# Kernel tuning notes

Measured on AMD Instinct MI355X. Metric: run time of the kernel, lower is better.

## Reference

```python
import jax, jax.numpy as jnp
import numpy as np

B, S, D, R, H = 4, 2048, 1024, 256, 8
NI, NP, NO, K = 8, 32, 8, 3
DH = R // H


def _householder_chain(x, vs):
    # x: [B,S,R], vs: [B,S,K,R]; apply K Householder reflections sequentially
    def step(carry, v):
        vn = v * jax.lax.rsqrt(jnp.sum(v * v, axis=-1, keepdims=True) + 1e-8)
        vTx = jnp.sum(carry * vn, axis=-1, keepdims=True)
        return carry - 2.0 * vn * vTx, None
    out, _ = jax.lax.scan(step, x, jnp.moveaxis(vs, 2, 0))
    return out


def _circuit_down(x, in_neurons, proc_neurons, input_weights, proc_idx):
    # soft mixture of input-neuron projections: d_model -> rank
    all_proj = jnp.einsum('bsd,ndr->bsnr', x, in_neurons)
    xr = jnp.einsum('bsnr,bsn->bsr', all_proj, input_weights)
    return _householder_chain(xr, proc_neurons[proc_idx])


def setup_inputs():
    key = jax.random.key(0)
    ks = jax.random.split(key, 14)
    n = lambda k, shape, sc: jax.random.normal(k, shape, jnp.float32) * sc
    inv_d, inv_r = 1.0 / np.sqrt(D), 1.0 / np.sqrt(R)
    return {
        'x': n(ks[0], (B, S, D), 1.0),
        'q_in': n(ks[1], (NI, D, R), inv_d),
        'q_proc': n(ks[2], (NP, R), inv_r),
        'k_in': n(ks[3], (NI, D, R), inv_d),
        'k_proc': n(ks[4], (NP, R), inv_r),
        'v_in': n(ks[5], (NI, D, R), inv_d),
        'v_proc': n(ks[6], (NP, R), inv_r),
        'o_proc': n(ks[7], (NP, R), inv_r),
        'o_out': n(ks[8], (NO, R, D), inv_r),
        'rd_in': n(ks[9], (NI, D), inv_d),
        'rd_proc': n(ks[10], (NP, D), inv_d),
        'ru_out': n(ks[11], (NO, R), inv_r),
        'ru_proc': n(ks[12], (NP, R), inv_r),
    }


def reference(x, q_in, q_proc, k_in, k_proc, v_in, v_proc, o_proc, o_out,
              rd_in, rd_proc, ru_out, ru_proc):
    # --- router (down): soft input weights + top-k process indices ---
    input_weights = jax.nn.softmax(x @ rd_in.T, axis=-1)          # [B,S,NI]
    _, pidx = jax.lax.top_k(x @ rd_proc.T, K)                     # [B,S,K]

    q = _circuit_down(x, q_in, q_proc, input_weights, pidx)      # [B,S,R]
    k = _circuit_down(x, k_in, k_proc, input_weights, pidx)
    v = _circuit_down(x, v_in, v_proc, input_weights, pidx)

    qh = q.reshape(B, S, H, DH)
    kh = k.reshape(B, S, H, DH)
    vh = v.reshape(B, S, H, DH)
    scores = jnp.einsum('bqhd,bkhd->bhqk', qh, kh) / np.sqrt(DH)
    attn = jax.nn.softmax(scores, axis=-1)
    o = jnp.einsum('bhqk,bkhd->bqhd', attn, vh).reshape(B, S, R)  # [B,S,R]

    # --- router (up): soft output weights + top-k process indices ---
    output_weights = jax.nn.softmax(o @ ru_out.T, axis=-1)        # [B,S,NO]
    _, pidx_u = jax.lax.top_k(o @ ru_proc.T, K)                   # [B,S,K]

    oh = _householder_chain(o, o_proc[pidx_u])                    # [B,S,R]
    out = jnp.einsum('bsr,bsn,nrd->bsd', oh, output_weights, o_out)
    return out
```

## Files before the change

kernel.cpp:

```cpp
#include <hip/hip_runtime.h>
#include <math.h>

#define NI 8
#define NP 32
#define TOPK 3

typedef _Float16 f16;
typedef f16 f16x8 __attribute__((ext_vector_type(8)));
typedef f16 f16x4 __attribute__((ext_vector_type(4)));
typedef float f32x4 __attribute__((ext_vector_type(4)));

__device__ __forceinline__ float wave_sum(float v) {
  #pragma unroll
  for (int off = 32; off; off >>= 1) v += __shfl_xor(v, off);
  return v;
}

__device__ __forceinline__ unsigned int pack_f16x2(float x) {
  f16 h = (f16)x;
  f16 l = (f16)(x - (float)h);
  return (unsigned int)__builtin_bit_cast(unsigned short, h)
       | ((unsigned int)__builtin_bit_cast(unsigned short, l) << 16);
}

__device__ __forceinline__ void unpack8(const unsigned int* p, f16x8& hi, f16x8& lo) {
  uint4 w0 = *reinterpret_cast<const uint4*>(p);
  uint4 w1 = *reinterpret_cast<const uint4*>(p + 4);
  union { unsigned int u[4]; f16x8 v; } H, L;
  H.u[0] = (w0.x & 0xffffu) | (w0.y << 16);
  L.u[0] = (w0.x >> 16)     | (w0.y & 0xffff0000u);
  H.u[1] = (w0.z & 0xffffu) | (w0.w << 16);
  L.u[1] = (w0.z >> 16)     | (w0.w & 0xffff0000u);
  H.u[2] = (w1.x & 0xffffu) | (w1.y << 16);
  L.u[2] = (w1.x >> 16)     | (w1.y & 0xffff0000u);
  H.u[3] = (w1.z & 0xffffu) | (w1.w << 16);
  L.u[3] = (w1.z >> 16)     | (w1.w & 0xffff0000u);
  hi = H.v; lo = L.v;
}

template<int CHUNKS>
__global__ __launch_bounds__(256) void router_kernel(
    const float* __restrict__ X,
    const float* __restrict__ Wsm,
    const float* __restrict__ Wtk,
    float* __restrict__ iw, int* __restrict__ pidx)
{
  const int tid = threadIdx.x, wave = tid >> 6, lane = tid & 63;
  const int t = blockIdx.x * 4 + wave;
  __shared__ float sc[4][40];
  const int Kin = CHUNKS * 256;
  const float4* Xp = reinterpret_cast<const float4*>(X + (size_t)t * Kin);
  float4 xv[CHUNKS];
  #pragma unroll
  for (int c = 0; c < CHUNKS; ++c) xv[c] = Xp[c * 64 + lane];

  for (int w = 0; w < 40; ++w) {
    const float* Wr = (w < NI) ? (Wsm + (size_t)w * Kin) : (Wtk + (size_t)(w - NI) * Kin);
    const float4* Wp = reinterpret_cast<const float4*>(Wr);
    float p = 0.f;
    #pragma unroll
    for (int c = 0; c < CHUNKS; ++c) {
      float4 wv = Wp[c * 64 + lane];
      p = fmaf(xv[c].x, wv.x, p); p = fmaf(xv[c].y, wv.y, p);
      p = fmaf(xv[c].z, wv.z, p); p = fmaf(xv[c].w, wv.w, p);
    }
    p = wave_sum(p);
    if (lane == 0) sc[wave][w] = p;
  }
  float s = (lane < NI) ? sc[wave][lane] : -3.0e38f;
  float m = s;
  #pragma unroll
  for (int off = 4; off; off >>= 1) m = fmaxf(m, __shfl_xor(m, off));
  float e = expf(s - m);
  float sum = e;
  #pragma unroll
  for (int off = 4; off; off >>= 1) sum += __shfl_xor(sum, off);
  if (lane < NI) iw[(size_t)t * NI + lane] = e / sum;

  float v = (lane < NP) ? sc[wave][NI + lane] : -3.0e38f;
  int idx = lane;
  #pragma unroll
  for (int j = 0; j < TOPK; ++j) {
    float bv = v; int bi = idx;
    #pragma unroll
    for (int off = 32; off; off >>= 1) {
      float ov = __shfl_xor(bv, off); int oi = __shfl_xor(bi, off);
      if (ov > bv || (ov == bv && oi < bi)) { bv = ov; bi = oi; }
    }
    if (lane == 0) pidx[t * TOPK + j] = bi;
    if (idx == bi) v = -3.0e38f;
  }
}

__global__ __launch_bounds__(256) void pack_bt(
    const float* __restrict__ S, f16* __restrict__ Dh, f16* __restrict__ Dl,
    int C, int K)
{
  __shared__ float T[64][65];
  const int tid = threadIdx.x;
  const int kb = blockIdx.x * 64, cb = blockIdx.y * 64;
  const int tr = tid >> 4, tc = (tid & 15) * 4;
  #pragma unroll
  for (int i = 0; i < 4; ++i) {
    float4 v = *reinterpret_cast<const float4*>(&S[(size_t)(kb + tr + i * 16) * C + cb + tc]);
    T[tr + i * 16][tc + 0] = v.x; T[tr + i * 16][tc + 1] = v.y;
    T[tr + i * 16][tc + 2] = v.z; T[tr + i * 16][tc + 3] = v.w;
  }
  __syncthreads();
  #pragma unroll
  for (int i = 0; i < 4; ++i) {
    int c = tr + i * 16;
    f16x4 vh, vl;
    #pragma unroll
    for (int q = 0; q < 4; ++q) {
      float a = T[tc + q][c];
      f16 h = (f16)a;
      vh[q] = h;
      vl[q] = (f16)(a - (float)h);
    }
    *reinterpret_cast<f16x4*>(&Dh[(size_t)(cb + c) * K + kb + tc]) = vh;
    *reinterpret_cast<f16x4*>(&Dl[(size_t)(cb + c) * K + kb + tc]) = vl;
  }
}

#define SBM 128
#define SBN 64
#define SBK 32

__global__ __launch_bounds__(256, 3) void gemm_split(
    const float* __restrict__ X, int Kin,
    const float* __restrict__ W,
    const f16* __restrict__ Bth, const f16* __restrict__ Btl,
    float* __restrict__ C, int ldC, int Ktot)
{
  __shared__ f16x8 AhU[SBM * 4];
  __shared__ f16x8 AlU[SBM * 4];
  __shared__ f16x8 BhU[SBN * 4];
  __shared__ f16x8 BlU[SBN * 4];
  __shared__ float Ws[SBM][NI];

  const int tid = threadIdx.x;
  const int row0 = blockIdx.x * SBM;
  const int c0 = blockIdx.y * SBN;

  const int wave = tid >> 6, lane = tid & 63;
  const int wm = wave >> 1, wn = wave & 1;
  const int fr = lane & 15, ks = lane >> 4;

  for (int i = tid; i < SBM * NI; i += 256)
    Ws[i >> 3][i & 7] = W[(size_t)(row0 + (i >> 3)) * NI + (i & 7)];

  const int arow = tid >> 1, ahalf = tid & 1;
  const float* xrow = X + (size_t)(row0 + arow) * Kin + ahalf * 16;
  const int bcol = tid >> 2;
  const int bks = (tid & 3) ^ (bcol & 3);
  const f16* bsh = Bth + (size_t)(c0 + bcol) * Ktot + bks * 8;
  const f16* bsl = Btl + (size_t)(c0 + bcol) * Ktot + bks * 8;

  f32x4 acc[4][2] = {};

  int n = 0, dk0 = 0;
  for (int kt = 0; kt < Ktot; kt += SBK) {
    __syncthreads();
    {
      float4 v0 = *reinterpret_cast<const float4*>(xrow + dk0);
      float4 v1 = *reinterpret_cast<const float4*>(xrow + dk0 + 4);
      float4 v2 = *reinterpret_cast<const float4*>(xrow + dk0 + 8);
      float4 v3 = *reinterpret_cast<const float4*>(xrow + dk0 + 12);
      float wgt = Ws[arow][n];
      float a[16] = {v0.x, v0.y, v0.z, v0.w, v1.x, v1.y, v1.z, v1.w,
                     v2.x, v2.y, v2.z, v2.w, v3.x, v3.y, v3.z, v3.w};
      f16x8 h0, h1, l0, l1;
      #pragma unroll
      for (int j = 0; j < 8; ++j) {
        float p0 = a[j] * wgt, p1 = a[8 + j] * wgt;
        f16 hh0 = (f16)p0, hh1 = (f16)p1;
        h0[j] = hh0; l0[j] = (f16)(p0 - (float)hh0);
        h1[j] = hh1; l1[j] = (f16)(p1 - (float)hh1);
      }
      const int sw = arow & 3;
      AhU[arow * 4 + ((ahalf * 2 + 0) ^ sw)] = h0;
      AhU[arow * 4 + ((ahalf * 2 + 1) ^ sw)] = h1;
      AlU[arow * 4 + ((ahalf * 2 + 0) ^ sw)] = l0;
      AlU[arow * 4 + ((ahalf * 2 + 1) ^ sw)] = l1;
      BhU[tid] = *reinterpret_cast<const f16x8*>(bsh + kt);
      BlU[tid] = *reinterpret_cast<const f16x8*>(bsl + kt);
    }
    __syncthreads();
    f16x8 ah[4], al[4], bh[2], bl[2];
    #pragma unroll
    for (int mf = 0; mf < 4; ++mf) {
      int ar = wm * 64 + mf * 16 + fr;
      int s = ar * 4 + (ks ^ (ar & 3));
      ah[mf] = AhU[s]; al[mf] = AlU[s];
    }
    #pragma unroll
    for (int nf = 0; nf < 2; ++nf) {
      int bc = wn * 32 + nf * 16 + fr;
      int s = bc * 4 + (ks ^ (bc & 3));
      bh[nf] = BhU[s]; bl[nf] = BlU[s];
    }
    #pragma unroll
    for (int mf = 0; mf < 4; ++mf)
      #pragma unroll
      for (int nf = 0; nf < 2; ++nf) {
        acc[mf][nf] = __builtin_amdgcn_mfma_f32_16x16x32_f16(ah[mf], bh[nf], acc[mf][nf], 0, 0, 0);
        acc[mf][nf] = __builtin_amdgcn_mfma_f32_16x16x32_f16(ah[mf], bl[nf], acc[mf][nf], 0, 0, 0);
        acc[mf][nf] = __builtin_amdgcn_mfma_f32_16x16x32_f16(al[mf], bh[nf], acc[mf][nf], 0, 0, 0);
      }
    dk0 += SBK;
    if (dk0 == Kin) { dk0 = 0; ++n; }
  }
  #pragma unroll
  for (int mf = 0; mf < 4; ++mf)
    #pragma unroll
    for (int nf = 0; nf < 2; ++nf) {
      int col = c0 + wn * 32 + nf * 16 + fr;
      #pragma unroll
      for (int j = 0; j < 4; ++j) {
        int row = row0 + wm * 64 + mf * 16 + ks * 4 + j;
        C[(size_t)row * ldC + col] = acc[mf][nf][j];
      }
    }
}

#define GBM 128
#define GBN 128
#define GBK 16
#define GBMp 132

__global__ __launch_bounds__(256) void gemm_mix(
    const float* __restrict__ X, int Kin,
    const float* __restrict__ W,
    const float* __restrict__ Bm0, const float* __restrict__ Bm1, const float* __restrict__ Bm2,
    int ldB, float* __restrict__ C, int ldC, int Nz)
{
  __shared__ float As[GBK][GBMp];
  __shared__ float Bs[GBK][GBMp];
  __shared__ float Ws[GBM][NI];
  const int tid = threadIdx.x;
  const int row0 = blockIdx.x * GBM;
  const int z = blockIdx.z;
  const float* Bm = (z == 0) ? Bm0 : (z == 1) ? Bm1 : Bm2;
  const int c0 = blockIdx.y * GBN;
  for (int i = tid; i < GBM * NI; i += 256)
    Ws[i >> 3][i & 7] = W[(size_t)(row0 + (i >> 3)) * NI + (i & 7)];
  __syncthreads();

  float acc[8][8] = {};
  const int tr = tid >> 4, tc = tid & 15;
  const int srow = tid >> 2;
  const int sseg = (tid & 3) * 4;
  const int bk = tid >> 4;
  const int bc = (tid & 15) * 4;

  const int Ktot = Kin * NI;
  int n = 0, dk0 = 0;
  for (int kt = 0; kt < Ktot; kt += GBK) {
    __syncthreads();
    #pragma unroll
    for (int p = 0; p < 2; ++p) {
      int r = p * 64 + srow;
      float4 xv = *reinterpret_cast<const float4*>(&X[(size_t)(row0 + r) * Kin + dk0 + sseg]);
      float wgt = Ws[r][n];
      As[sseg + 0][r] = xv.x * wgt;
      As[sseg + 1][r] = xv.y * wgt;
      As[sseg + 2][r] = xv.z * wgt;
      As[sseg + 3][r] = xv.w * wgt;
    }
    #pragma unroll
    for (int p = 0; p < 2; ++p) {
      int cc = p * 64 + bc;
      float4 bv = *reinterpret_cast<const float4*>(&Bm[(size_t)(kt + bk) * ldB + c0 + cc]);
      *reinterpret_cast<float4*>(&Bs[bk][cc]) = bv;
    }
    __syncthreads();
    #pragma unroll
    for (int k = 0; k < GBK; ++k) {
      float4 a0 = *reinterpret_cast<const float4*>(&As[k][tr * 8]);
      float4 a1 = *reinterpret_cast<const float4*>(&As[k][tr * 8 + 4]);
      float4 b0 = *reinterpret_cast<const float4*>(&Bs[k][tc * 8]);
      float4 b1 = *reinterpret_cast<const float4*>(&Bs[k][tc * 8 + 4]);
      float av[8] = {a0.x, a0.y, a0.z, a0.w, a1.x, a1.y, a1.z, a1.w};
      float bv[8] = {b0.x, b0.y, b0.z, b0.w, b1.x, b1.y, b1.z, b1.w};
      #pragma unroll
      for (int i = 0; i < 8; ++i)
        #pragma unroll
        for (int j = 0; j < 8; ++j)
          acc[i][j] = fmaf(av[i], bv[j], acc[i][j]);
    }
    dk0 += GBK;
    if (dk0 == Kin) { dk0 = 0; ++n; }
  }
  #pragma unroll
  for (int i = 0; i < 8; ++i) {
    int row = row0 + tr * 8 + i;
    float* Cp = C + (size_t)row * ldC + z * Nz + c0 + tc * 8;
    float4 o0 = {acc[i][0], acc[i][1], acc[i][2], acc[i][3]};
    float4 o1 = {acc[i][4], acc[i][5], acc[i][6], acc[i][7]};
    *reinterpret_cast<float4*>(Cp) = o0;
    *reinterpret_cast<float4*>(Cp + 4) = o1;
  }
}

__global__ __launch_bounds__(256) void hh_kernel(
    float* __restrict__ X, int ldX,
    const float* __restrict__ P0, const float* __restrict__ P1, const float* __restrict__ P2,
    const int* __restrict__ pidx)
{
  const int tid = threadIdx.x, wave = tid >> 6, lane = tid & 63;
  const int t = blockIdx.x * 4 + wave;
  const int circ = blockIdx.y;
  const float* P = (circ == 0) ? P0 : (circ == 1) ? P1 : P2;
  float* xp = X + (size_t)t * ldX + circ * 256;
  float4 x4 = *reinterpret_cast<float4*>(xp + lane * 4);
  #pragma unroll
  for (int j = 0; j < TOPK; ++j) {
    int id = pidx[t * TOPK + j];
    const float* vp = P + (size_t)id * 256;
    float4 v4 = *reinterpret_cast<const float4*>(vp + lane * 4);
    float ss = v4.x * v4.x + v4.y * v4.y + v4.z * v4.z + v4.w * v4.w;
    ss = wave_sum(ss);
    float inv = 1.0f / sqrtf(ss + 1e-8f);
    float4 vn = {v4.x * inv, v4.y * inv, v4.z * inv, v4.w * inv};
    float dt = vn.x * x4.x + vn.y * x4.y + vn.z * x4.z + vn.w * x4.w;
    dt = wave_sum(dt);
    float d2 = 2.0f * dt;
    x4.x = fmaf(-d2, vn.x, x4.x);
    x4.y = fmaf(-d2, vn.y, x4.y);
    x4.z = fmaf(-d2, vn.z, x4.z);
    x4.w = fmaf(-d2, vn.w, x4.w);
  }
  *reinterpret_cast<float4*>(xp + lane * 4) = x4;
}

__global__ __launch_bounds__(256, 2) void attn_mfma(
    const float* __restrict__ qkv, float* __restrict__ O)
{
  __shared__ f16 Kh[64][40];
  __shared__ f16 Kl[64][40];
  __shared__ unsigned int Vtp[32][68];
  __shared__ unsigned int Pp[4][32][68];

  const int tid = threadIdx.x, wave = tid >> 6, lane = tid & 63;
  const int c = lane & 15, g = lane >> 4;
  const int bh = blockIdx.y, b = bh >> 3, h = bh & 7;
  const int q0 = blockIdx.x * 128;
  const size_t tbase = (size_t)b * 2048;
  const float SCALE = 0.17677669529663687f;

  f16x8 qh[2], ql[2];
  #pragma unroll
  for (int qt = 0; qt < 2; ++qt) {
    const int row = q0 + wave * 32 + qt * 16 + c;
    const float* qp = qkv + (tbase + row) * 768 + h * 32 + g * 8;
    float4 a = *reinterpret_cast<const float4*>(qp);
    float4 b4 = *reinterpret_cast<const float4*>(qp + 4);
    float qv[8] = {a.x, a.y, a.z, a.w, b4.x, b4.y, b4.z, b4.w};
    #pragma unroll
    for (int j = 0; j < 8; ++j) {
      float xs = qv[j] * SCALE;
      f16 hh = (f16)xs;
      qh[qt][j] = hh;
      ql[qt][j] = (f16)(xs - (float)hh);
    }
  }

  f32x4 sacc[2][4];
  f32x4 oacc[2][2] = {};
  float mrow[2][4] = {{-INFINITY, -INFINITY, -INFINITY, -INFINITY},
                      {-INFINITY, -INFINITY, -INFINITY, -INFINITY}};
  float lrow[2][4] = {};

  for (int k0 = 0; k0 < 2048; k0 += 64) {
    __syncthreads();
    {
      const int kj = tid >> 2, dq = (tid & 3) * 8;
      const float* kp = qkv + (tbase + k0 + kj) * 768 + 256 + h * 32 + dq;
      float4 ka = *reinterpret_cast<const float4*>(kp);
      float4 kb = *reinterpret_cast<const float4*>(kp + 4);
      float kv[8] = {ka.x, ka.y, ka.z, ka.w, kb.x, kb.y, kb.z, kb.w};
      f16x8 khi, klo;
      #pragma unroll
      for (int j = 0; j < 8; ++j) {
        f16 hh = (f16)kv[j];
        khi[j] = hh;
        klo[j] = (f16)(kv[j] - (float)hh);
      }
      *reinterpret_cast<f16x8*>(&Kh[kj][dq]) = khi;
      *reinterpret_cast<f16x8*>(&Kl[kj][dq]) = klo;

      const int vk = tid & 63, vq = (tid >> 6) * 8;
      const float* vp = qkv + (tbase + k0 + vk) * 768 + 512 + h * 32 + vq;
      float4 va = *reinterpret_cast<const float4*>(vp);
      float4 vb = *reinterpret_cast<const float4*>(vp + 4);
      float vv[8] = {va.x, va.y, va.z, va.w, vb.x, vb.y, vb.z, vb.w};
      #pragma unroll
      for (int j = 0; j < 8; ++j) Vtp[vq + j][vk] = pack_f16x2(vv[j]);
    }
    __syncthreads();

    #pragma unroll
    for (int s = 0; s < 4; ++s) {
      f16x8 kbh = *reinterpret_cast<const f16x8*>(&Kh[s * 16 + c][g * 8]);
      f16x8 kbl = *reinterpret_cast<const f16x8*>(&Kl[s * 16 + c][g * 8]);
      #pragma unroll
      for (int qt = 0; qt < 2; ++qt) {
        f32x4 acc = {0.f, 0.f, 0.f, 0.f};
        acc = __builtin_amdgcn_mfma_f32_16x16x32_f16(qh[qt], kbh, acc, 0, 0, 0);
        acc = __builtin_amdgcn_mfma_f32_16x16x32_f16(qh[qt], kbl, acc, 0, 0, 0);
        acc = __builtin_amdgcn_mfma_f32_16x16x32_f16(ql[qt], kbh, acc, 0, 0, 0);
        sacc[qt][s] = acc;
      }
    }

    float alpha[2][4];
    #pragma unroll
    for (int qt = 0; qt < 2; ++qt)
      #pragma unroll
      for (int r = 0; r < 4; ++r) {
        float mt = fmaxf(fmaxf(sacc[qt][0][r], sacc[qt][1][r]),
                         fmaxf(sacc[qt][2][r], sacc[qt][3][r]));
        #pragma unroll
        for (int off = 1; off < 16; off <<= 1) mt = fmaxf(mt, __shfl_xor(mt, off));
        float mn = fmaxf(mrow[qt][r], mt);
        float al = __expf(mrow[qt][r] - mn);
        mrow[qt][r] = mn;
        alpha[qt][r] = al;
        float ps = 0.f;
        #pragma unroll
        for (int s = 0; s < 4; ++s) {
          float p = __expf(sacc[qt][s][r] - mn);
          sacc[qt][s][r] = p;
          ps += p;
        }
        #pragma unroll
        for (int off = 1; off < 16; off <<= 1) ps += __shfl_xor(ps, off);
        lrow[qt][r] = lrow[qt][r] * al + ps;
      }

    #pragma unroll
    for (int qt = 0; qt < 2; ++qt)
      #pragma unroll
      for (int s = 0; s < 4; ++s)
        #pragma unroll
        for (int r = 0; r < 4; ++r)
          Pp[wave][qt * 16 + g * 4 + r][s * 16 + c] = pack_f16x2(sacc[qt][s][r]);

    #pragma unroll
    for (int qt = 0; qt < 2; ++qt)
      #pragma unroll
      for (int dh = 0; dh < 2; ++dh)
        #pragma unroll
        for (int r = 0; r < 4; ++r) oacc[qt][dh][r] *= alpha[qt][r];

    #pragma unroll
    for (int ch = 0; ch < 2; ++ch) {
      f16x8 pah[2], pal[2];
      #pragma unroll
      for (int qt = 0; qt < 2; ++qt)
        unpack8(&Pp[wave][qt * 16 + c][ch * 32 + g * 8], pah[qt], pal[qt]);
      #pragma unroll
      for (int dh = 0; dh < 2; ++dh) {
        f16x8 vh, vl;
        unpack8(&Vtp[dh * 16 + c][ch * 32 + g * 8], vh, vl);
        #pragma unroll
        for (int qt = 0; qt < 2; ++qt) {
          oacc[qt][dh] = __builtin_amdgcn_mfma_f32_16x16x32_f16(pah[qt], vh, oacc[qt][dh], 0, 0, 0);
          oacc[qt][dh] = __builtin_amdgcn_mfma_f32_16x16x32_f16(pah[qt], vl, oacc[qt][dh], 0, 0, 0);
          oacc[qt][dh] = __builtin_amdgcn_mfma_f32_16x16x32_f16(pal[qt], vh, oacc[qt][dh], 0, 0, 0);
        }
      }
    }
  }

  #pragma unroll
  for (int qt = 0; qt < 2; ++qt)
    #pragma unroll
    for (int r = 0; r < 4; ++r) {
      float inv = 1.0f / lrow[qt][r];
      int row = q0 + wave * 32 + qt * 16 + g * 4 + r;
      #pragma unroll
      for (int dh = 0; dh < 2; ++dh)
        O[(tbase + row) * 256 + h * 32 + dh * 16 + c] = oacc[qt][dh][r] * inv;
    }
}

__global__ __launch_bounds__(256) void attn_kernel(
    const float* __restrict__ qkv, float* __restrict__ O)
{
  const int tid = threadIdx.x;
  const int wave = tid >> 6, lane = tid & 63;
  const int bh = blockIdx.y, b = bh >> 3, h = bh & 7;
  const int q0 = blockIdx.x * 8;
  const size_t tbase = (size_t)b * 2048;
  const float SCALE = 0.17677669529663687f;

  __shared__ float Ks[64][36];
  __shared__ float Vt[32][68];
  __shared__ float Ps[4][2][64];

  const int wq = __builtin_amdgcn_readfirstlane(wave);
  const float* qr0 = qkv + (tbase + q0 + wq * 2) * 768 + h * 32;
  float qa[32], qb[32];
  #pragma unroll
  for (int i = 0; i < 32; ++i) { qa[i] = qr0[i]; qb[i] = qr0[768 + i]; }

  const int r = lane >> 5, d = lane & 31;
  float m0 = -INFINITY, m1 = -INFINITY, l0 = 0.f, l1 = 0.f, oacc = 0.f;

  for (int k0 = 0; k0 < 2048; k0 += 64) {
    __syncthreads();
    {
      int j = tid >> 2;
      int c = (tid & 3) * 8;
      const float* kp = qkv + (tbase + k0 + j) * 768 + 256 + h * 32 + c;
      float4 ka = *reinterpret_cast<const float4*>(kp);
      float4 kb = *reinterpret_cast<const float4*>(kp + 4);
      *reinterpret_cast<float4*>(&Ks[j][c]) = ka;
      *reinterpret_cast<float4*>(&Ks[j][c + 4]) = kb;
      const float* vp = qkv + (tbase + k0 + j) * 768 + 512 + h * 32 + c;
      float4 va = *reinterpret_cast<const float4*>(vp);
      float4 vb = *reinterpret_cast<const float4*>(vp + 4);
      Vt[c + 0][j] = va.x; Vt[c + 1][j] = va.y; Vt[c + 2][j] = va.z; Vt[c + 3][j] = va.w;
      Vt[c + 4][j] = vb.x; Vt[c + 5][j] = vb.y; Vt[c + 6][j] = vb.z; Vt[c + 7][j] = vb.w;
    }
    __syncthreads();
    float s0 = 0.f, s1 = 0.f;
    #pragma unroll
    for (int dd = 0; dd < 8; ++dd) {
      float4 kv = *reinterpret_cast<const float4*>(&Ks[lane][dd * 4]);
      s0 = fmaf(qa[dd * 4 + 0], kv.x, s0); s1 = fmaf(qb[dd * 4 + 0], kv.x, s1);
      s0 = fmaf(qa[dd * 4 + 1], kv.y, s0); s1 = fmaf(qb[dd * 4 + 1], kv.y, s1);
      s0 = fmaf(qa[dd * 4 + 2], kv.z, s0); s1 = fmaf(qb[dd * 4 + 2], kv.z, s1);
      s0 = fmaf(qa[dd * 4 + 3], kv.w, s0); s1 = fmaf(qb[dd * 4 + 3], kv.w, s1);
    }
    s0 *= SCALE; s1 *= SCALE;
    float mx0 = s0, mx1 = s1;
    #pragma unroll
    for (int off = 32; off; off >>= 1) {
      mx0 = fmaxf(mx0, __shfl_xor(mx0, off));
      mx1 = fmaxf(mx1, __shfl_xor(mx1, off));
    }
    float nm0 = fmaxf(m0, mx0), nm1 = fmaxf(m1, mx1);
    float p0 = expf(s0 - nm0), p1 = expf(s1 - nm1);
    float a0 = expf(m0 - nm0), a1 = expf(m1 - nm1);
    float sp0 = p0, sp1 = p1;
    #pragma unroll
    for (int off = 32; off; off >>= 1) {
      sp0 += __shfl_xor(sp0, off);
      sp1 += __shfl_xor(sp1, off);
    }
    l0 = l0 * a0 + sp0; l1 = l1 * a1 + sp1;
    m0 = nm0; m1 = nm1;
    Ps[wave][0][lane] = p0; Ps[wave][1][lane] = p1;
    oacc *= (r == 0) ? a0 : a1;
    #pragma unroll
    for (int jq = 0; jq < 16; ++jq) {
      float4 pv = *reinterpret_cast<const float4*>(&Ps[wave][r][jq * 4]);
      float4 vv = *reinterpret_cast<const float4*>(&Vt[d][jq * 4]);
      oacc = fmaf(pv.x, vv.x, oacc);
      oacc = fmaf(pv.y, vv.y, oacc);
      oacc = fmaf(pv.z, vv.z, oacc);
      oacc = fmaf(pv.w, vv.w, oacc);
    }
  }
  float lf = (r == 0) ? l0 : l1;
  oacc /= lf;
  O[(tbase + q0 + wave * 2 + r) * 256 + h * 32 + d] = oacc;
}

extern "C" void kernel_launch(void* const* d_in, const int* in_sizes, int n_in,
                              void* d_out, int out_size, void* d_ws, size_t ws_size,
                              hipStream_t stream) {
  const float* x       = (const float*)d_in[0];
  const float* q_in    = (const float*)d_in[1];
  const float* q_proc  = (const float*)d_in[2];
  const float* k_in    = (const float*)d_in[3];
  const float* k_proc  = (const float*)d_in[4];
  const float* v_in    = (const float*)d_in[5];
  const float* v_proc  = (const float*)d_in[6];
  const float* o_proc  = (const float*)d_in[7];
  const float* o_out   = (const float*)d_in[8];
  const float* rd_in   = (const float*)d_in[9];
  const float* rd_proc = (const float*)d_in[10];
  const float* ru_out  = (const float*)d_in[11];
  const float* ru_proc = (const float*)d_in[12];
  float* out = (float*)d_out;
  float* qkv = (float*)d_out;

  const size_t NEED = (768ull << 10) + 768ull * 8192 * 2 * 2;

  if (ws_size >= NEED) {
    char* wsb = (char*)d_ws;
    float* iw    = (float*)wsb;
    float* owt   = (float*)(wsb + (256 << 10));
    int*   pidx  = (int*)(wsb + (512 << 10));
    int*   pidxu = (int*)(wsb + (640 << 10));
    char*  Xr    = wsb + (768 << 10);
    f16* bth_q = (f16*)Xr;
    f16* btl_q = (f16*)(Xr + 768ull * 8192 * 2);
    float* obuf = (float*)Xr;
    f16* bth_o = (f16*)(Xr + (8ull << 20));
    f16* btl_o = (f16*)(Xr + (8ull << 20) + 1024ull * 2048 * 2);

    router_kernel<4><<<dim3(2048), dim3(256), 0, stream>>>(x, rd_in, rd_proc, iw, pidx);
    pack_bt<<<dim3(128, 4), dim3(256), 0, stream>>>(q_in, bth_q,                btl_q,                256, 8192);
    pack_bt<<<dim3(128, 4), dim3(256), 0, stream>>>(k_in, bth_q + 256ull * 8192, btl_q + 256ull * 8192, 256, 8192);
    pack_bt<<<dim3(128, 4), dim3(256), 0, stream>>>(v_in, bth_q + 512ull * 8192, btl_q + 512ull * 8192, 256, 8192);
    gemm_split<<<dim3(64, 12), dim3(256), 0, stream>>>(x, 1024, iw, bth_q, btl_q, qkv, 768, 8192);
    hh_kernel<<<dim3(2048, 3), dim3(256), 0, stream>>>(qkv, 768, q_proc, k_proc, v_proc, pidx);
    pack_bt<<<dim3(32, 16), dim3(256), 0, stream>>>(o_out, bth_o, btl_o, 1024, 2048);
    attn_mfma<<<dim3(16, 32), dim3(256), 0, stream>>>(qkv, obuf);
    router_kernel<1><<<dim3(2048), dim3(256), 0, stream>>>(obuf, ru_out, ru_proc, owt, pidxu);
    hh_kernel<<<dim3(2048, 1), dim3(256), 0, stream>>>(obuf, 256, o_proc, o_proc, o_proc, pidxu);
    gemm_split<<<dim3(64, 16), dim3(256), 0, stream>>>(obuf, 256, owt, bth_o, btl_o, out, 1024, 2048);
  } else {
    float* ws = (float*)d_ws;
    float* iw    = ws;
    int*   pidx  = (int*)(ws + 65536);
    float* obuf  = ws + 65536 + 24576;
    float* owt   = obuf + 8192 * 256;
    int*   pidxu = (int*)(owt + 65536);

    router_kernel<4><<<dim3(2048), dim3(256), 0, stream>>>(x, rd_in, rd_proc, iw, pidx);
    gemm_mix<<<dim3(64, 2, 3), dim3(256), 0, stream>>>(x, 1024, iw, q_in, k_in, v_in,
                                                       256, qkv, 768, 256);
    hh_kernel<<<dim3(2048, 3), dim3(256), 0, stream>>>(qkv, 768, q_proc, k_proc, v_proc, pidx);
    attn_kernel<<<dim3(256, 32), dim3(256), 0, stream>>>(qkv, obuf);
    router_kernel<1><<<dim3(2048), dim3(256), 0, stream>>>(obuf, ru_out, ru_proc, owt, pidxu);
    hh_kernel<<<dim3(2048, 1), dim3(256), 0, stream>>>(obuf, 256, o_proc, o_proc, o_proc, pidxu);
    gemm_mix<<<dim3(64, 8, 1), dim3(256), 0, stream>>>(obuf, 256, owt, o_out, o_out, o_out,
                                                       1024, out, 1024, 1024);
  }
}
```

Before: 823.6 us.

## Pre-split activations to f16 hi/lo and use async LDS-load GEMM with larger tiles

```diff
diff --git a/kernel.cpp b/kernel.cpp
--- a/kernel.cpp
+++ b/kernel.cpp
@@ -14,6 +14,12 @@
   #pragma unroll
   for (int off = 32; off; off >>= 1) v += __shfl_xor(v, off);
   return v;
+}
+
+__device__ __forceinline__ void gload16(const void* g, void* l) {
+  __builtin_amdgcn_global_load_lds(
+      (const __attribute__((address_space(1))) unsigned int*)g,
+      (__attribute__((address_space(3))) unsigned int*)l, 16, 0, 0);
 }
 
 __device__ __forceinline__ unsigned int pack_f16x2(float x) {
@@ -121,6 +127,143 @@
     *reinterpret_cast<f16x4*>(&Dh[(size_t)(cb + c) * K + kb + tc]) = vh;
     *reinterpret_cast<f16x4*>(&Dl[(size_t)(cb + c) * K + kb + tc]) = vl;
   }
+}
+
+__global__ __launch_bounds__(256) void pack_split(
+    const float* __restrict__ S, f16* __restrict__ Dh, f16* __restrict__ Dl,
+    size_t n8)
+{
+  size_t i = ((size_t)blockIdx.x * 256 + threadIdx.x);
+  if (i >= n8) return;
+  const float* s = S + i * 8;
+  float4 a = *reinterpret_cast<const float4*>(s);
+  float4 b = *reinterpret_cast<const float4*>(s + 4);
+  float v[8] = {a.x, a.y, a.z, a.w, b.x, b.y, b.z, b.w};
+  f16x8 h, l;
+  #pragma unroll
+  for (int j = 0; j < 8; ++j) {
+    f16 hh = (f16)v[j];
+    h[j] = hh;
+    l[j] = (f16)(v[j] - (float)hh);
+  }
+  *reinterpret_cast<f16x8*>(Dh + i * 8) = h;
+  *reinterpret_cast<f16x8*>(Dl + i * 8) = l;
+}
+
+#define TBM 128
+#define TBN 128
+#define TBK 32
+
+__global__ __launch_bounds__(256, 2) void gemm_split2(
+    const f16* __restrict__ Xh, const f16* __restrict__ Xl, int Kin,
+    const float* __restrict__ W,
+    const f16* __restrict__ Bth, const f16* __restrict__ Btl,
+    float* __restrict__ C, int ldC, int Ktot)
+{
+  __shared__ f16x8 AhL[512];
+  __shared__ f16x8 AlL[512];
+  __shared__ f16x8 BhL[512];
+  __shared__ f16x8 BlL[512];
+  __shared__ float Ws[TBM][NI];
+
+  const int tid = threadIdx.x;
+  const int wave = tid >> 6, lane = tid & 63;
+  const int wm = wave >> 1, wn = wave & 1;
+  const int fr = lane & 15, ks = lane >> 4;
+  const int row0 = blockIdx.x * TBM, c0 = blockIdx.y * TBN;
+
+  for (int i = tid; i < TBM * NI; i += 256)
+    Ws[i >> 3][i & 7] = W[(size_t)(row0 + (i >> 3)) * NI + (i & 7)];
+
+  const int s1 = 256 + tid;
+  const int ar0 = tid >> 2, kg0 = ((tid & 3) - (ar0 >> 1)) & 3;
+  const int ar1 = s1 >> 2,  kg1 = ((s1 & 3) - (ar1 >> 1)) & 3;
+
+  const f16* xh0 = Xh + (size_t)(row0 + ar0) * Kin + kg0 * 8;
+  const f16* xh1 = Xh + (size_t)(row0 + ar1) * Kin + kg1 * 8;
+  const f16* xl0 = Xl + (size_t)(row0 + ar0) * Kin + kg0 * 8;
+  const f16* xl1 = Xl + (size_t)(row0 + ar1) * Kin + kg1 * 8;
+  const f16* bh0 = Bth + (size_t)(c0 + ar0) * Ktot + kg0 * 8;
+  const f16* bh1 = Bth + (size_t)(c0 + ar1) * Ktot + kg1 * 8;
+  const f16* bl0 = Btl + (size_t)(c0 + ar0) * Ktot + kg0 * 8;
+  const f16* bl1 = Btl + (size_t)(c0 + ar1) * Ktot + kg1 * 8;
+
+  f16x8* AhW = &AhL[wave * 64];
+  f16x8* AlW = &AlL[wave * 64];
+  f16x8* BhW = &BhL[wave * 64];
+  f16x8* BlW = &BlL[wave * 64];
+
+  f32x4 acc[4][4] = {};
+  f32x4 cac[4][4] = {};
+
+  int n = 0, dk0 = 0;
+  for (int kt = 0; kt < Ktot; kt += TBK) {
+    __syncthreads();
+    gload16(xh0 + dk0, AhW);
+    gload16(xh1 + dk0, AhW + 256);
+    gload16(xl0 + dk0, AlW);
+    gload16(xl1 + dk0, AlW + 256);
+    gload16(bh0 + kt, BhW);
+    gload16(bh1 + kt, BhW + 256);
+    gload16(bl0 + kt, BlW);
+    gload16(bl1 + kt, BlW + 256);
+    __syncthreads();
+
+    f16x8 ah[4], al[4], bh[4], bl[4];
+    #pragma unroll
+    for (int mf = 0; mf < 4; ++mf) {
+      int ar = wm * 64 + mf * 16 + fr;
+      int sl = ar * 4 + (((ar >> 1) + ks) & 3);
+      ah[mf] = AhL[sl]; al[mf] = AlL[sl];
+    }
+    #pragma unroll
+    for (int nf = 0; nf < 4; ++nf) {
+      int bc = wn * 64 + nf * 16 + fr;
+      int sl = bc * 4 + (((bc >> 1) + ks) & 3);
+      bh[nf] = BhL[sl]; bl[nf] = BlL[sl];
+    }
+    #pragma unroll
+    for (int mf = 0; mf < 4; ++mf)
+      #pragma unroll
+      for (int nf = 0; nf < 4; ++nf) {
+        acc[mf][nf] = __builtin_amdgcn_mfma_f32_16x16x32_f16(ah[mf], bh[nf], acc[mf][nf], 0, 0, 0);
+        acc[mf][nf] = __builtin_amdgcn_mfma_f32_16x16x32_f16(ah[mf], bl[nf], acc[mf][nf], 0, 0, 0);
+        acc[mf][nf] = __builtin_amdgcn_mfma_f32_16x16x32_f16(al[mf], bh[nf], acc[mf][nf], 0, 0, 0);
+      }
+
+    dk0 += TBK;
+    if (dk0 == Kin) {
+      dk0 = 0;
+      #pragma unroll
+      for (int mf = 0; mf < 4; ++mf) {
+        float w0 = Ws[wm * 64 + mf * 16 + ks * 4 + 0][n];
+        float w1 = Ws[wm * 64 + mf * 16 + ks * 4 + 1][n];
+        float w2 = Ws[wm * 64 + mf * 16 + ks * 4 + 2][n];
+        float w3 = Ws[wm * 64 + mf * 16 + ks * 4 + 3][n];
+        #pragma unroll
+        for (int nf = 0; nf < 4; ++nf) {
+          cac[mf][nf][0] = fmaf(w0, acc[mf][nf][0], cac[mf][nf][0]);
+          cac[mf][nf][1] = fmaf(w1, acc[mf][nf][1], cac[mf][nf][1]);
+          cac[mf][nf][2] = fmaf(w2, acc[mf][nf][2], cac[mf][nf][2]);
+          cac[mf][nf][3] = fmaf(w3, acc[mf][nf][3], cac[mf][nf][3]);
+          acc[mf][nf] = (f32x4){0.f, 0.f, 0.f, 0.f};
+        }
+      }
+      ++n;
+    }
+  }
+
+  #pragma unroll
+  for (int mf = 0; mf < 4; ++mf)
+    #pragma unroll
+    for (int nf = 0; nf < 4; ++nf) {
+      int col = c0 + wn * 64 + nf * 16 + fr;
+      #pragma unroll
+      for (int j = 0; j < 4; ++j) {
+        int row = row0 + wm * 64 + mf * 16 + ks * 4 + j;
+        C[(size_t)row * ldC + col] = cac[mf][nf][j];
+      }
+    }
 }
 
 #define SBM 128
@@ -589,9 +732,42 @@
   float* out = (float*)d_out;
   float* qkv = (float*)d_out;
 
-  const size_t NEED = (768ull << 10) + 768ull * 8192 * 2 * 2;
-
-  if (ws_size >= NEED) {
+  const size_t NEED  = (768ull << 10) + 768ull * 8192 * 2 * 2;
+  const size_t NEED2 = (768ull << 10) + 768ull * 8192 * 2 * 2
+                     + 8192ull * 1024 * 2 * 2;
+
+  if (ws_size >= NEED2) {
+    char* wsb = (char*)d_ws;
+    float* iw    = (float*)wsb;
+    float* owt   = (float*)(wsb + (256 << 10));
+    int*   pidx  = (int*)(wsb + (512 << 10));
+    int*   pidxu = (int*)(wsb + (640 << 10));
+    char*  R1    = wsb + (768 << 10);
+    f16* bth_q = (f16*)R1;
+    f16* btl_q = (f16*)(R1 + 768ull * 8192 * 2);
+    char*  R2    = R1 + 768ull * 8192 * 2 * 2;
+    f16* Xh = (f16*)R2;
+    f16* Xl = (f16*)(R2 + 8192ull * 1024 * 2);
+    float* obuf = (float*)R2;
+    f16* Oh    = (f16*)(R2 + (8192ull * 256 * 4));
+    f16* Ol    = (f16*)(R2 + (8192ull * 256 * 4) + 8192ull * 256 * 2);
+    f16* bth_o = (f16*)(R2 + (8192ull * 256 * 4) + 8192ull * 256 * 2 * 2);
+    f16* btl_o = (f16*)(R2 + (8192ull * 256 * 4) + 8192ull * 256 * 2 * 2 + 2048ull * 1024 * 2);
+
+    router_kernel<4><<<dim3(2048), dim3(256), 0, stream>>>(x, rd_in, rd_proc, iw, pidx);
+    pack_split<<<dim3(4096), dim3(256), 0, stream>>>(x, Xh, Xl, 8192ull * 1024 / 8);
+    pack_bt<<<dim3(128, 4), dim3(256), 0, stream>>>(q_in, bth_q,                 btl_q,                 256, 8192);
+    pack_bt<<<dim3(128, 4), dim3(256), 0, stream>>>(k_in, bth_q + 256ull * 8192, btl_q + 256ull * 8192, 256, 8192);
+    pack_bt<<<dim3(128, 4), dim3(256), 0, stream>>>(v_in, bth_q + 512ull * 8192, btl_q + 512ull * 8192, 256, 8192);
+    gemm_split2<<<dim3(64, 6), dim3(256), 0, stream>>>(Xh, Xl, 1024, iw, bth_q, btl_q, qkv, 768, 8192);
+    hh_kernel<<<dim3(2048, 3), dim3(256), 0, stream>>>(qkv, 768, q_proc, k_proc, v_proc, pidx);
+    pack_bt<<<dim3(32, 16), dim3(256), 0, stream>>>(o_out, bth_o, btl_o, 1024, 2048);
+    attn_mfma<<<dim3(16, 32), dim3(256), 0, stream>>>(qkv, obuf);
+    router_kernel<1><<<dim3(2048), dim3(256), 0, stream>>>(obuf, ru_out, ru_proc, owt, pidxu);
+    hh_kernel<<<dim3(2048, 1), dim3(256), 0, stream>>>(obuf, 256, o_proc, o_proc, o_proc, pidxu);
+    pack_split<<<dim3(1024), dim3(256), 0, stream>>>(obuf, Oh, Ol, 8192ull * 256 / 8);
+    gemm_split2<<<dim3(64, 8), dim3(256), 0, stream>>>(Oh, Ol, 256, owt, bth_o, btl_o, out, 1024, 2048);
+  } else if (ws_size >= NEED) {
     char* wsb = (char*)d_ws;
     float* iw    = (float*)wsb;
     float* owt   = (float*)(wsb + (256 << 10));
@@ -605,7 +781,7 @@
     f16* btl_o = (f16*)(Xr + (8ull << 20) + 1024ull * 2048 * 2);
 
     router_kernel<4><<<dim3(2048), dim3(256), 0, stream>>>(x, rd_in, rd_proc, iw, pidx);
-    pack_bt<<<dim3(128, 4), dim3(256), 0, stream>>>(q_in, bth_q,                btl_q,                256, 8192);
+    pack_bt<<<dim3(128, 4), dim3(256), 0, stream>>>(q_in, bth_q,                 btl_q,                 256, 8192);
     pack_bt<<<dim3(128, 4), dim3(256), 0, stream>>>(k_in, bth_q + 256ull * 8192, btl_q + 256ull * 8192, 256, 8192);
     pack_bt<<<dim3(128, 4), dim3(256), 0, stream>>>(v_in, bth_q + 512ull * 8192, btl_q + 512ull * 8192, 256, 8192);
     gemm_split<<<dim3(64, 12), dim3(256), 0, stream>>>(x, 1024, iw, bth_q, btl_q, qkv, 768, 8192);
```

After: 702.3 us. 14.7% less time.
